# Optimization experiments

Hardware: AMD Instinct MI355X
Metric: run time of the kernel (lower is better)

## Reference

```python
import jax, jax.numpy as jnp
import numpy as np

DIM = 768      # model dim
NH = 12        # num heads
WS = 32        # window/input size (H = W = WS)
B = 8          # batch


def _relative_position_index(ws):
    # Mirrors the torch buffer construction.
    coords = np.stack(np.meshgrid(np.arange(ws), np.arange(ws), indexing='ij'))  # [2, ws, ws]
    cf = coords.reshape(2, -1)                                # [2, N]
    rel = cf[:, :, None] - cf[:, None, :]                     # [2, N, N]
    rel = rel.transpose(1, 2, 0).astype(np.int64)             # [N, N, 2]
    rel[..., 0] += ws - 1
    rel[..., 1] += ws - 1
    rel[..., 0] *= 2 * ws - 1
    return rel.sum(-1)                                        # [N, N]


def setup_inputs() -> dict:
    key = jax.random.key(0)
    ks = jax.random.split(key, 5)
    std = 0.02
    x = jax.random.normal(ks[0], (B, WS, WS, DIM), jnp.float32)
    qkv_w = jax.random.normal(ks[1], (3 * DIM, DIM), jnp.float32) * std
    q_bias = jnp.zeros((DIM,), jnp.float32)
    v_bias = jnp.zeros((DIM,), jnp.float32)
    proj_w = jax.random.normal(ks[2], (DIM, DIM), jnp.float32) * std
    proj_b = jnp.zeros((DIM,), jnp.float32)
    num_rel = (2 * WS - 1) * (2 * WS - 1) + 3
    rel_table = jax.random.normal(ks[3], (num_rel, NH), jnp.float32) * std
    rel_index = jnp.asarray(_relative_position_index(WS), jnp.int32)
    return {
        'x': x, 'qkv_w': qkv_w, 'q_bias': q_bias, 'v_bias': v_bias,
        'proj_w': proj_w, 'proj_b': proj_b, 'rel_table': rel_table,
        'rel_index': rel_index,
    }


def reference(x, qkv_w, q_bias, v_bias, proj_w, proj_b, rel_table, rel_index):
    Bb, H, W, C = x.shape
    N = H * W
    hd = C // NH
    scale = hd ** (-0.5)
    # qkv bias: [q_bias, zeros(k), v_bias]
    qkv_b = jnp.concatenate([q_bias, jnp.zeros_like(v_bias), v_bias])
    qkv = x.reshape(Bb, N, C) @ qkv_w.T + qkv_b                # [B, N, 3C]
    qkv = qkv.reshape(Bb, N, 3, NH, hd).transpose(2, 0, 3, 1, 4)  # [3, B, nh, N, hd]
    q, k, v = qkv[0] * scale, qkv[1], qkv[2]
    attn = jnp.einsum('bhqd,bhkd->bhqk', q, k)                 # [B, nh, N, N]
    bias = rel_table[rel_index.reshape(-1)].reshape(N, N, NH)  # [N, N, nh]
    bias = bias.transpose(2, 0, 1)                             # [nh, N, N]
    attn = jax.nn.softmax(attn + bias[None], axis=-1)
    out = jnp.einsum('bhqk,bhkd->bhqd', attn, v)               # [B, nh, N, hd]
    out = out.transpose(0, 2, 1, 3).reshape(Bb, H, W, C)
    return out @ proj_w.T + proj_b
```

## Files before the change

kernel.cpp:

```cpp
#include <hip/hip_runtime.h>
#include <cstdint>
#include <cstddef>

#define DIMC 768
#define NHH  12
#define NSEQ 1024
#define HD   64

#define SX  6291456
#define SW1 1769472
#define SW2 589824

#define RELN 3969
#define RELP 4032

typedef _Float16 f16x8 __attribute__((ext_vector_type(8)));
typedef _Float16 f16x4 __attribute__((ext_vector_type(4)));
typedef float    f32x4 __attribute__((ext_vector_type(4)));
typedef float    f32x16 __attribute__((ext_vector_type(16)));
typedef float    f32x4u __attribute__((ext_vector_type(4), aligned(4)));

__device__ inline void gld16(const _Float16* g, _Float16* l) {
  __builtin_amdgcn_global_load_lds(
      (const __attribute__((address_space(1))) void*)g,
      (__attribute__((address_space(3))) void*)l, 16, 0, 0);
}

__global__ __launch_bounds__(256) void cast_f16(
    const float* __restrict__ x, const float* __restrict__ w1,
    const float* __restrict__ w2, _Float16* __restrict__ dst) {
  const long long t = (long long)blockIdx.x * 256 + threadIdx.x;
  const long long i = t * 8;
  const float* src; long long off;
  if (i < SX) { src = x; off = i; }
  else if (i < SX + SW1) { src = w1; off = i - SX; }
  else { src = w2; off = i - (SX + SW1); }
  const float4 a = *(const float4*)(src + off);
  const float4 b = *(const float4*)(src + off + 4);
  f16x8 o;
  o[0] = (_Float16)a.x; o[1] = (_Float16)a.y; o[2] = (_Float16)a.z; o[3] = (_Float16)a.w;
  o[4] = (_Float16)b.x; o[5] = (_Float16)b.y; o[6] = (_Float16)b.z; o[7] = (_Float16)b.w;
  *(f16x8*)(dst + i) = o;
}

template <int EPI>
__global__ __launch_bounds__(256) void gemm_mfma(
    const _Float16* __restrict__ A, const _Float16* __restrict__ W,
    const float* __restrict__ b0, const float* __restrict__ b1,
    float* __restrict__ outF, _Float16* __restrict__ oq,
    _Float16* __restrict__ ok, _Float16* __restrict__ ovt) {
  __shared__ _Float16 Alds[128 * 32];
  __shared__ _Float16 Blds[128 * 32];

  const int tid = threadIdx.x;
  const int w = tid >> 6, lane = tid & 63, quad = lane >> 4, l16 = lane & 15;
  const int m0 = (blockIdx.x & 63) << 7;
  const int o0 = (blockIdx.x >> 6) << 7;
  const int wr = (w >> 1) * 64, wc = (w & 1) * 64;

  f32x4 acc[4][4];
#pragma unroll
  for (int i = 0; i < 4; i++)
#pragma unroll
    for (int j = 0; j < 4; j++) acc[i][j] = (f32x4){0.f, 0.f, 0.f, 0.f};

  const int c0 = tid, c1 = 256 + tid;
  const int r0 = c0 >> 2, cb0 = (c0 & 3) * 8;
  const int r1 = c1 >> 2, cb1 = (c1 & 3) * 8;
  const _Float16* Ap0 = A + (size_t)(m0 + r0) * DIMC + cb0;
  const _Float16* Ap1 = A + (size_t)(m0 + r1) * DIMC + cb1;
  const _Float16* Wp0 = W + (size_t)(o0 + r0) * DIMC + cb0;
  const _Float16* Wp1 = W + (size_t)(o0 + r1) * DIMC + cb1;

  for (int k0 = 0; k0 < DIMC; k0 += 32) {
    __syncthreads();
    gld16(Ap0 + k0, &Alds[c0 * 8]);
    gld16(Ap1 + k0, &Alds[c1 * 8]);
    gld16(Wp0 + k0, &Blds[c0 * 8]);
    gld16(Wp1 + k0, &Blds[c1 * 8]);
    __syncthreads();

    f16x8 a[4], b[4];
#pragma unroll
    for (int i = 0; i < 4; i++)
      a[i] = *(const f16x8*)&Alds[(wr + i * 16 + l16) * 32 + quad * 8];
#pragma unroll
    for (int j = 0; j < 4; j++)
      b[j] = *(const f16x8*)&Blds[(wc + j * 16 + l16) * 32 + quad * 8];
#pragma unroll
    for (int i = 0; i < 4; i++)
#pragma unroll
      for (int j = 0; j < 4; j++)
        acc[i][j] = __builtin_amdgcn_mfma_f32_16x16x32_f16(a[i], b[j], acc[i][j], 0, 0, 0);
  }

  if constexpr (EPI == 0) {
#pragma unroll
    for (int j = 0; j < 4; j++) {
      const int o = o0 + wc + j * 16 + l16;
      const int part = o / DIMC;
      const int cc = o - part * DIMC;
      const int hh = cc >> 6, d = cc & 63;
      const float badd = (part == 0) ? b0[cc] : (part == 2 ? b1[cc] : 0.f);
      if (part == 2) {
#pragma unroll
        for (int i = 0; i < 4; i++) {
          const int mb = m0 + wr + i * 16 + quad * 4;
          const int bb = mb >> 10, n0 = mb & 1023;
          f16x4 vv;
#pragma unroll
          for (int r = 0; r < 4; r++) vv[r] = (_Float16)(acc[i][j][r] + badd);
          *(f16x4*)(ovt + (((size_t)(bb * NHH + hh)) * HD + d) * NSEQ + n0) = vv;
        }
      } else {
        _Float16* dst = (part == 0) ? oq : ok;
#pragma unroll
        for (int i = 0; i < 4; i++) {
#pragma unroll
          for (int r = 0; r < 4; r++) {
            const int m = m0 + wr + i * 16 + quad * 4 + r;
            const int bb = m >> 10, n = m & 1023;
            float v = acc[i][j][r];
            if (part == 0) v = (v + badd) * 0.125f;
            dst[(((size_t)(bb * NHH + hh)) * NSEQ + n) * HD + d] = (_Float16)v;
          }
        }
      }
    }
  } else {
#pragma unroll
    for (int j = 0; j < 4; j++) {
      const int o = o0 + wc + j * 16 + l16;
      const float bo = b0[o];
#pragma unroll
      for (int i = 0; i < 4; i++) {
#pragma unroll
        for (int r = 0; r < 4; r++) {
          const int m = m0 + wr + i * 16 + quad * 4 + r;
          outF[(size_t)m * DIMC + o] = acc[i][j][r] + bo;
        }
      }
    }
  }
}

__global__ __launch_bounds__(256) void relt_pre(const float* __restrict__ rel_table,
                                                float* __restrict__ relT) {
  const int g = blockIdx.x * 256 + threadIdx.x;
  if (g >= NHH * RELN) return;
  const int h = g / RELN, idx = g - h * RELN;
  relT[h * RELP + idx] = rel_table[idx * NHH + h];
}

__global__ __launch_bounds__(256, 3) void flash_mfma(
    const _Float16* __restrict__ Qg, const _Float16* __restrict__ Kg,
    const _Float16* __restrict__ Vtg, const float* __restrict__ relT,
    _Float16* __restrict__ AO) {
  const int nblk = blockIdx.x;
  const int bhl = nblk % 96;
  const int qt = nblk / 96;
  const int head = bhl >> 3, b = bhl & 7;
  const int bh = b * NHH + head;
  const int tid = threadIdx.x, w = tid >> 6, lane = tid & 63;
  const int ql = lane & 31;
  const int hf = lane >> 5;

  __shared__ _Float16 Klds[128 * 64];
  __shared__ _Float16 Vlds[64 * 128];

  const int qglob = qt * 128 + w * 32 + ql;
  const _Float16* Qrow = Qg + ((size_t)bh * NSEQ + qglob) * HD + hf * 8;
  f16x8 bq[4];
#pragma unroll
  for (int s = 0; s < 4; s++) bq[s] = *(const f16x8*)(Qrow + s * 16);

  f32x16 O0 = {}, O1 = {};
  float psum = 0.f;

  const _Float16* Kbase = Kg + (size_t)bh * NSEQ * HD;
  const _Float16* Vtbase = Vtg + (size_t)bh * HD * NSEQ;

  const float* relTh = relT + (size_t)head * RELP;
  const int qy = qt * 4 + w;
  const int idxb = ql + 31 - 4 * hf;

  const int vrow0 = ql, vrow1 = 32 + ql;
  const int vkey0 = (vrow0 ^ (vrow0 >> 3)) & 7;
  const int vkey1 = (vrow1 ^ (vrow1 >> 3)) & 7;

  for (int kt = 0; kt < 8; kt++) {
    __syncthreads();
#pragma unroll
    for (int c4 = 0; c4 < 4; c4++) {
      const int c = tid + c4 * 256;
      const int kr = c >> 3, kc = c & 7;
      const int kpos = (kr << 3) | (kc ^ ((kr ^ (kr >> 3)) & 7));
      *(f16x8*)&Klds[kpos * 8] =
          *(const f16x8*)(Kbase + ((size_t)(kt * 128 + kr)) * HD + kc * 8);
      const int vr = c >> 4, vc = c & 15;
      const int vpos = (vr << 4) | (vc ^ ((vr ^ (vr >> 3)) & 7));
      *(f16x8*)&Vlds[vpos * 8] =
          *(const f16x8*)(Vtbase + (size_t)vr * NSEQ + kt * 128 + vc * 8);
    }
    __syncthreads();

#pragma unroll
    for (int t = 0; t < 4; t++) {
      const int arow = t * 32 + ql;
      const int akey = (arow ^ (arow >> 3)) & 7;
      f32x16 S = {};
#pragma unroll
      for (int s = 0; s < 4; s++) {
        const f16x8 ak = *(const f16x8*)&Klds[((arow << 3) | ((s * 2 + hf) ^ akey)) * 8];
        S = __builtin_amdgcn_mfma_f32_32x32x16_f16(ak, bq[s], S, 0, 0, 0);
      }

      const float* rowb = relTh + (qy - (kt * 4 + t) + 31) * 63 + idxb;
      unsigned int dw[8];
#pragma unroll
      for (int g = 0; g < 4; g++) {
        const f32x4u bv = *(const f32x4u*)(rowb - 8 * g - 3);
        const float p0 = __expf(S[4 * g + 0] + bv[3]);
        const float p1 = __expf(S[4 * g + 1] + bv[2]);
        const float p2 = __expf(S[4 * g + 2] + bv[1]);
        const float p3 = __expf(S[4 * g + 3] + bv[0]);
        psum += (p0 + p1) + (p2 + p3);
        union { f16x4 h; unsigned int u[2]; } cv;
        cv.h[0] = (_Float16)p0; cv.h[1] = (_Float16)p1;
        cv.h[2] = (_Float16)p2; cv.h[3] = (_Float16)p3;
        dw[2 * g] = cv.u[0]; dw[2 * g + 1] = cv.u[1];
      }

#pragma unroll
      for (int s = 0; s < 2; s++) {
        const unsigned int x0 = hf ? dw[4 * s + 0] : dw[4 * s + 2];
        const unsigned int x1 = hf ? dw[4 * s + 1] : dw[4 * s + 3];
        const unsigned int y0 = (unsigned int)__shfl_xor((int)x0, 32, 64);
        const unsigned int y1 = (unsigned int)__shfl_xor((int)x1, 32, 64);
        union { unsigned int u[4]; f16x8 v; } bp;
        if (hf == 0) {
          bp.u[0] = dw[4 * s + 0]; bp.u[1] = dw[4 * s + 1];
          bp.u[2] = y0;            bp.u[3] = y1;
        } else {
          bp.u[0] = y0;            bp.u[1] = y1;
          bp.u[2] = dw[4 * s + 2]; bp.u[3] = dw[4 * s + 3];
        }
        const int kchunk = t * 4 + s * 2 + hf;
        const f16x8 av0 = *(const f16x8*)&Vlds[((vrow0 << 4) | (kchunk ^ vkey0)) * 8];
        O0 = __builtin_amdgcn_mfma_f32_32x32x16_f16(av0, bp.v, O0, 0, 0, 0);
        const f16x8 av1 = *(const f16x8*)&Vlds[((vrow1 << 4) | (kchunk ^ vkey1)) * 8];
        O1 = __builtin_amdgcn_mfma_f32_32x32x16_f16(av1, bp.v, O1, 0, 0, 0);
      }
    }
  }

  psum += __shfl_xor(psum, 32, 64);
  const float inv = 1.f / psum;
  _Float16* aoRow = AO + ((size_t)(b * NSEQ + qglob)) * DIMC + head * HD;
#pragma unroll
  for (int g = 0; g < 4; g++) {
    f16x4 o0, o1;
#pragma unroll
    for (int j = 0; j < 4; j++) {
      o0[j] = (_Float16)(O0[4 * g + j] * inv);
      o1[j] = (_Float16)(O1[4 * g + j] * inv);
    }
    const int d0 = 8 * g + 4 * hf;
    *(f16x4*)(aoRow + d0) = o0;
    *(f16x4*)(aoRow + 32 + d0) = o1;
  }
}

extern "C" void kernel_launch(void* const* d_in, const int* in_sizes, int n_in,
                              void* d_out, int out_size, void* d_ws, size_t ws_size,
                              hipStream_t stream) {
  const float* x        = (const float*)d_in[0];
  const float* qkv_w    = (const float*)d_in[1];
  const float* q_bias   = (const float*)d_in[2];
  const float* v_bias   = (const float*)d_in[3];
  const float* proj_w   = (const float*)d_in[4];
  const float* proj_b   = (const float*)d_in[5];
  const float* rel_tab  = (const float*)d_in[6];
  float* out = (float*)d_out;

  const size_t NTOK = (size_t)8 * NHH * NSEQ * HD;
  _Float16* Xb     = (_Float16*)d_ws;
  _Float16* Wqkvb  = Xb + SX;
  _Float16* Wprojb = Wqkvb + SW1;
  _Float16* Qb     = Wprojb + SW2;
  _Float16* Kb     = Qb + NTOK;
  _Float16* Vt     = Kb + NTOK;
  float*    relT   = (float*)(Vt + NTOK);
  _Float16* AOb    = Xb;

  cast_f16<<<dim3((SX + SW1 + SW2) / 2048), 256, 0, stream>>>(x, qkv_w, proj_w, Xb);

  relt_pre<<<dim3((NHH * RELN + 255) / 256), 256, 0, stream>>>(rel_tab, relT);

  gemm_mfma<0><<<dim3(64 * 18), 256, 0, stream>>>(
      Xb, Wqkvb, q_bias, v_bias, nullptr, Qb, Kb, Vt);

  flash_mfma<<<dim3(768), 256, 0, stream>>>(Qb, Kb, Vt, relT, AOb);

  gemm_mfma<1><<<dim3(64 * 6), 256, 0, stream>>>(
      AOb, Wprojb, proj_b, nullptr, out, nullptr, nullptr, nullptr);
}
```

Baseline: 234.8 us.

## Prefetch next K/V tile into registers and double-buffer bias loads in attention

The attention loop now issues global loads for the next K and V^T tile into registers right after the LDS barrier, so they overlap with the current tile's MFMA work, and only copies registers to LDS at the start of each iteration. Relative-position bias rows are loaded one sub-tile ahead into a two-slot register buffer, and the LDS swizzle offsets are precomputed once. s_setprio is raised around the MFMA sections to favour matrix issue. This raises register pressure, which may lower occupancy, and the last bias prefetch reads a row past the final sub-tile.

```diff
diff --git a/kernel.cpp b/kernel.cpp
--- a/kernel.cpp
+++ b/kernel.cpp
@@ -188,38 +188,74 @@
   const int vkey0 = (vrow0 ^ (vrow0 >> 3)) & 7;
   const int vkey1 = (vrow1 ^ (vrow1 >> 3)) & 7;
 
+  int kof[4], vof[4], kpa[4], vpa[4];
+#pragma unroll
+  for (int c4 = 0; c4 < 4; c4++) {
+    const int c = tid + c4 * 256;
+    const int kr = c >> 3, kc = c & 7;
+    kof[c4] = kr * HD + kc * 8;
+    kpa[c4] = (((kr << 3) | (kc ^ ((kr ^ (kr >> 3)) & 7)))) * 8;
+    const int vr = c >> 4, vc = c & 15;
+    vof[c4] = vr * NSEQ + vc * 8;
+    vpa[c4] = (((vr << 4) | (vc ^ ((vr ^ (vr >> 3)) & 7)))) * 8;
+  }
+
+  f16x8 kreg[4], vreg[4];
+#pragma unroll
+  for (int c4 = 0; c4 < 4; c4++) {
+    kreg[c4] = *(const f16x8*)(Kbase + kof[c4]);
+    vreg[c4] = *(const f16x8*)(Vtbase + vof[c4]);
+  }
+
+  f32x4u bvp[2][4];
+  {
+    const float* rowb0 = relTh + (qy + 31) * 63 + idxb;
+#pragma unroll
+    for (int g = 0; g < 4; g++) bvp[0][g] = *(const f32x4u*)(rowb0 - 8 * g - 3);
+  }
+
   for (int kt = 0; kt < 8; kt++) {
     __syncthreads();
 #pragma unroll
     for (int c4 = 0; c4 < 4; c4++) {
-      const int c = tid + c4 * 256;
-      const int kr = c >> 3, kc = c & 7;
-      const int kpos = (kr << 3) | (kc ^ ((kr ^ (kr >> 3)) & 7));
-      *(f16x8*)&Klds[kpos * 8] =
-          *(const f16x8*)(Kbase + ((size_t)(kt * 128 + kr)) * HD + kc * 8);
-      const int vr = c >> 4, vc = c & 15;
-      const int vpos = (vr << 4) | (vc ^ ((vr ^ (vr >> 3)) & 7));
-      *(f16x8*)&Vlds[vpos * 8] =
-          *(const f16x8*)(Vtbase + (size_t)vr * NSEQ + kt * 128 + vc * 8);
+      *(f16x8*)&Klds[kpa[c4]] = kreg[c4];
+      *(f16x8*)&Vlds[vpa[c4]] = vreg[c4];
     }
     __syncthreads();
 
+    if (kt < 7) {
+#pragma unroll
+      for (int c4 = 0; c4 < 4; c4++) {
+        kreg[c4] = *(const f16x8*)(Kbase + (kt + 1) * 128 * HD + kof[c4]);
+        vreg[c4] = *(const f16x8*)(Vtbase + (kt + 1) * 128 + vof[c4]);
+      }
+    }
+
 #pragma unroll
     for (int t = 0; t < 4; t++) {
+      {
+        const int taun = 4 * kt + t + 1;
+        const float* rowbn = relTh + (qy + 31 - taun) * 63 + idxb;
+#pragma unroll
+        for (int g = 0; g < 4; g++)
+          bvp[(t + 1) & 1][g] = *(const f32x4u*)(rowbn - 8 * g - 3);
+      }
+
       const int arow = t * 32 + ql;
       const int akey = (arow ^ (arow >> 3)) & 7;
       f32x16 S = {};
+      __builtin_amdgcn_s_setprio(1);
 #pragma unroll
       for (int s = 0; s < 4; s++) {
         const f16x8 ak = *(const f16x8*)&Klds[((arow << 3) | ((s * 2 + hf) ^ akey)) * 8];
         S = __builtin_amdgcn_mfma_f32_32x32x16_f16(ak, bq[s], S, 0, 0, 0);
       }
-
-      const float* rowb = relTh + (qy - (kt * 4 + t) + 31) * 63 + idxb;
+      __builtin_amdgcn_s_setprio(0);
+
       unsigned int dw[8];
 #pragma unroll
       for (int g = 0; g < 4; g++) {
-        const f32x4u bv = *(const f32x4u*)(rowb - 8 * g - 3);
+        const f32x4u bv = bvp[t & 1][g];
         const float p0 = __expf(S[4 * g + 0] + bv[3]);
         const float p1 = __expf(S[4 * g + 1] + bv[2]);
         const float p2 = __expf(S[4 * g + 2] + bv[1]);
@@ -231,6 +267,7 @@
         dw[2 * g] = cv.u[0]; dw[2 * g + 1] = cv.u[1];
       }
 
+      __builtin_amdgcn_s_setprio(1);
 #pragma unroll
       for (int s = 0; s < 2; s++) {
         const unsigned int x0 = hf ? dw[4 * s + 0] : dw[4 * s + 2];
@@ -251,6 +288,7 @@
         const f16x8 av1 = *(const f16x8*)&Vlds[((vrow1 << 4) | (kchunk ^ vkey1)) * 8];
         O1 = __builtin_amdgcn_mfma_f32_32x32x16_f16(av1, bp.v, O1, 0, 0, 0);
       }
+      __builtin_amdgcn_s_setprio(0);
     }
   }
 
```

Result: slower. 326.9 us (+39.2%).
